# Kernel optimization log

Measured on AMD Instinct MI355X. Metric: run time of the kernel, lower is better.

## Reference

```python
import jax, jax.numpy as jnp
import numpy as np

B, C_COMB, HW_IN, HW_FEAT, N_POS, D_PROJ, OUT_HW = 32, 448, 32, 64, 4096, 100, 256


def setup_inputs() -> dict:
    key = jax.random.key(0)
    k1, k2, k3, k4 = jax.random.split(key, 4)
    return {
        "combined": jax.random.normal(k1, (B, C_COMB, HW_IN, HW_IN), dtype=jnp.float32),
        "proj_w": jax.random.normal(k2, (D_PROJ, C_COMB), dtype=jnp.float32),
        "proj_b": jnp.zeros((D_PROJ,), dtype=jnp.float32),
        "mean": jax.random.normal(k3, (D_PROJ, N_POS), dtype=jnp.float32),
        "inv_covariance": jax.random.normal(k4, (N_POS, D_PROJ, D_PROJ), dtype=jnp.float32),
        "norm_min": jnp.zeros((), dtype=jnp.float32),
        "norm_max": jnp.ones((), dtype=jnp.float32),
    }


def reference(combined, proj_w, proj_b, mean, inv_covariance, norm_min, norm_max):
    b = combined.shape[0]
    # F.interpolate(..., size=(64,64), mode='bilinear', align_corners=False)
    feats = jax.image.resize(combined, (b, C_COMB, HW_FEAT, HW_FEAT), method="bilinear")
    # permute to NHWC and flatten spatial -> [B, 4096, 448]
    feats = feats.transpose(0, 2, 3, 1).reshape(b, N_POS, C_COMB)
    # nn.Linear(channels, 100) -> [B, 4096, 100]
    feats = jnp.einsum("bnc,dc->bnd", feats, proj_w) + proj_b
    # per-pixel Mahalanobis quadratic form: diff_n^T @ Sigma_n^{-1} @ diff_n
    diff = feats - mean.T[None]                                  # [B, 4096, 100]
    dist = jnp.einsum("bnc,ncd,bnd->bn", diff, inv_covariance, diff)  # [B, 4096]
    anomaly_map = dist.reshape(b, 1, HW_FEAT, HW_FEAT)
    anomaly_map = (anomaly_map - norm_min) / (norm_max - norm_min + 1e-8)
    anomaly_map = jax.image.resize(anomaly_map, (b, 1, OUT_HW, OUT_HW), method="bilinear")
    return anomaly_map
```

## Files before the change

kernel.cpp:

```cpp
#include <hip/hip_runtime.h>

#define B_      32
#define C_COMB  448
#define N_POS_  4096
#define D_      100

typedef __attribute__((ext_vector_type(8))) short bf16x8;
typedef __attribute__((ext_vector_type(4))) float f32x4;

__device__ __forceinline__ unsigned short f2bf(float f) {
    unsigned u = __builtin_bit_cast(unsigned, f);
    u += 0x7FFFu + ((u >> 16) & 1u);
    return (unsigned short)(u >> 16);
}
__device__ __forceinline__ unsigned pack2bf(float a, float b) {
    return (unsigned)f2bf(a) | ((unsigned)f2bf(b) << 16);
}
__device__ __forceinline__ float bf2f(unsigned short h) {
    return __builtin_bit_cast(float, (unsigned)h << 16);
}
__device__ __forceinline__ float4 bf4_to_f4(uint2 u) {
    float4 r;
    r.x = __builtin_bit_cast(float, u.x << 16);
    r.y = __builtin_bit_cast(float, u.x & 0xffff0000u);
    r.z = __builtin_bit_cast(float, u.y << 16);
    r.w = __builtin_bit_cast(float, u.y & 0xffff0000u);
    return r;
}
__device__ __forceinline__ void async_copy16(const void* g, void* lds) {
    __builtin_amdgcn_global_load_lds(
        (const __attribute__((address_space(1))) unsigned int*)g,
        (__attribute__((address_space(3))) unsigned int*)lds, 16, 0, 0);
}
__device__ __forceinline__ bf16x8 pack8bf(float4 lo, float4 hi) {
    bf16x8 r;
    r[0] = (short)f2bf(lo.x); r[1] = (short)f2bf(lo.y);
    r[2] = (short)f2bf(lo.z); r[3] = (short)f2bf(lo.w);
    r[4] = (short)f2bf(hi.x); r[5] = (short)f2bf(hi.y);
    r[6] = (short)f2bf(hi.z); r[7] = (short)f2bf(hi.w);
    return r;
}

__global__ __launch_bounds__(256) void k_meanT(const float* __restrict__ mean,
                                               float* __restrict__ meanT) {
    int i = blockIdx.x * 256 + threadIdx.x;
    if (i < D_ * N_POS_) {
        int d = i >> 12;
        int n = i & 4095;
        meanT[n * D_ + d] = mean[i];
    }
}

__global__ __launch_bounds__(256) void k_combT(const float* __restrict__ comb,
                                               unsigned short* __restrict__ combT) {
    __shared__ float T_[64][65];
    const int pt = blockIdx.x;
    const int ct = blockIdx.y;
    const int b  = blockIdx.z;
    const int t  = threadIdx.x;
    const int c0 = ct * 64, p0 = pt * 64;

    const float4* comb4 = (const float4*)comb;
#pragma unroll
    for (int k = 0; k < 4; k++) {
        int e4 = t + 256 * k;
        int cc = e4 >> 4, p4 = e4 & 15;
        float4 v = comb4[(b * C_COMB + c0 + cc) * 256 + pt * 16 + p4];
        T_[cc][p4 * 4 + 0] = v.x;
        T_[cc][p4 * 4 + 1] = v.y;
        T_[cc][p4 * 4 + 2] = v.z;
        T_[cc][p4 * 4 + 3] = v.w;
    }
    __syncthreads();
#pragma unroll
    for (int k = 0; k < 4; k++) {
        int e4 = t + 256 * k;
        int pp = e4 >> 4, c4 = e4 & 15;
        float f0 = T_[c4 * 4 + 0][pp];
        float f1 = T_[c4 * 4 + 1][pp];
        float f2 = T_[c4 * 4 + 2][pp];
        float f3 = T_[c4 * 4 + 3][pp];
        size_t R = (size_t)(p0 + pp) * 32 + b;
        *(uint2*)(combT + R * C_COMB + c0 + c4 * 4) =
            make_uint2(pack2bf(f0, f1), pack2bf(f2, f3));
    }
}

__global__ __launch_bounds__(256) void k_proj(const unsigned short* __restrict__ combT,
                                              const float* __restrict__ W,
                                              const float* __restrict__ bias,
                                              unsigned short* __restrict__ p32b) {
    __shared__ unsigned short Bb[64 * C_COMB];
    __shared__ unsigned short Ab[D_ * 32];

    const int t = threadIdx.x;
    const int lane = t & 63, w = t >> 6;
    const int c = lane & 15, q = lane >> 4;
    const int R0 = blockIdx.x * 64;

    const unsigned short* gB = combT + (size_t)R0 * C_COMB;
#pragma unroll
    for (int k = 0; k < 14; k++) {
        int f4 = (k * 4 + w) * 64 + lane;
        async_copy16(gB + f4 * 8, Bb + f4 * 8);
    }

    f32x4 acc[7];
#pragma unroll
    for (int mt = 0; mt < 7; mt++) acc[mt] = (f32x4){0.f, 0.f, 0.f, 0.f};

    const float4* W4 = (const float4*)W;

    for (int kt = 0; kt < 14; kt++) {
        __syncthreads();
#pragma unroll
        for (int k = 0; k < 4; k++) {
            int e4 = t + 256 * k;
            if (e4 < 800) {
                int rr = e4 >> 3, c4 = e4 & 7;
                float4 v = W4[rr * 112 + kt * 8 + c4];
                *(uint2*)(Ab + rr * 32 + c4 * 4) =
                    make_uint2(pack2bf(v.x, v.y), pack2bf(v.z, v.w));
            }
        }
        __syncthreads();

        bf16x8 bfrag = *(const bf16x8*)(Bb + (w * 16 + c) * C_COMB + kt * 32 + q * 8);
#pragma unroll
        for (int mt = 0; mt < 7; mt++) {
            int r = mt * 16 + c;
            bf16x8 afrag;
            if (r < D_) afrag = *(const bf16x8*)(Ab + r * 32 + q * 8);
            else        afrag = (bf16x8){0,0,0,0,0,0,0,0};
            acc[mt] = __builtin_amdgcn_mfma_f32_16x16x32_bf16(afrag, bfrag, acc[mt], 0, 0, 0);
        }
    }

    const int R = R0 + w * 16 + c;
#pragma unroll
    for (int mt = 0; mt < 7; mt++) {
        int d0 = mt * 16 + q * 4;
        if (d0 < D_) {
            f32x4 a = acc[mt];
            float o0 = a[0] + bias[d0 + 0];
            float o1 = a[1] + bias[d0 + 1];
            float o2 = a[2] + bias[d0 + 2];
            float o3 = a[3] + bias[d0 + 3];
            *(uint2*)(p32b + (size_t)R * D_ + d0) =
                make_uint2(pack2bf(o0, o1), pack2bf(o2, o3));
        }
    }
}

__global__ __launch_bounds__(128) void k_mahal(const unsigned short* __restrict__ p32b,
                                               const float* __restrict__ meanT,
                                               const float* __restrict__ icov,
                                               float* __restrict__ gdist) {
    __shared__ float Mf[D_ * D_];
    __shared__ unsigned short dTb[B_ * 104];

    const int n = blockIdx.x;
    const int t = threadIdx.x;
    const int lane = t & 63, w = t >> 6;
    const int c = lane & 15, q = lane >> 4;

    const float* gM = icov + (size_t)n * (D_ * D_);
#pragma unroll
    for (int k = 0; k < 19; k++) {
        int f4 = k * 128 + w * 64 + lane;
        async_copy16(gM + f4 * 4, Mf + f4 * 4);
    }
    if (t < 68) {
        int f4 = 2432 + t;
        ((float4*)Mf)[f4] = ((const float4*)gM)[f4];
    }

    const int y = n >> 6, x = n & 63;
    float sy = 0.5f * y - 0.25f, sx = 0.5f * x - 0.25f;
    float y0f = floorf(sy), x0f = floorf(sx);
    float fy = sy - y0f, fx = sx - x0f;
    int iy0 = max((int)y0f, 0), iy1 = min((int)y0f + 1, 31);
    int ix0 = max((int)x0f, 0), ix1 = min((int)x0f + 1, 31);
    const float w00 = (1.f - fy) * (1.f - fx), w01 = (1.f - fy) * fx;
    const float w10 = fy * (1.f - fx),         w11 = fy * fx;
    const unsigned short* s00 = p32b + (size_t)(iy0 * 32 + ix0) * 3200;
    const unsigned short* s01 = p32b + (size_t)(iy0 * 32 + ix1) * 3200;
    const unsigned short* s10 = p32b + (size_t)(iy1 * 32 + ix0) * 3200;
    const unsigned short* s11 = p32b + (size_t)(iy1 * 32 + ix1) * 3200;

    const float4* mt4 = (const float4*)meanT + n * 25;
#pragma unroll
    for (int k = 0; k < 7; k++) {
        int e4 = t + 128 * k;
        if (e4 < 800) {
            int b  = e4 / 25;
            int d4 = e4 - b * 25;
            float4 f00 = bf4_to_f4(*(const uint2*)(s00 + e4 * 4));
            float4 f01 = bf4_to_f4(*(const uint2*)(s01 + e4 * 4));
            float4 f10 = bf4_to_f4(*(const uint2*)(s10 + e4 * 4));
            float4 f11 = bf4_to_f4(*(const uint2*)(s11 + e4 * 4));
            float4 m = mt4[d4];
            float vx = w00 * f00.x + w01 * f01.x + w10 * f10.x + w11 * f11.x - m.x;
            float vy = w00 * f00.y + w01 * f01.y + w10 * f10.y + w11 * f11.y - m.y;
            float vz = w00 * f00.z + w01 * f01.z + w10 * f10.z + w11 * f11.z - m.z;
            float vw = w00 * f00.w + w01 * f01.w + w10 * f10.w + w11 * f11.w - m.w;
            *(uint2*)(dTb + b * 104 + d4 * 4) =
                make_uint2(pack2bf(vx, vy), pack2bf(vz, vw));
        }
    }
    if (t < 32) *(uint2*)(dTb + t * 104 + 100) = make_uint2(0u, 0u);

    __syncthreads();

    const int bb = w * 16 + c;
    f32x4 acc[7];
#pragma unroll
    for (int mt = 0; mt < 7; mt++) acc[mt] = (f32x4){0.f, 0.f, 0.f, 0.f};

#pragma unroll
    for (int kt = 0; kt < 4; kt++) {
        int k0 = kt * 32 + q * 8;
        bf16x8 bfrag;
        if (k0 < 104) bfrag = *(const bf16x8*)(dTb + bb * 104 + k0);
        else          bfrag = (bf16x8){0,0,0,0,0,0,0,0};
#pragma unroll
        for (int mt = 0; mt < 7; mt++) {
            int r = mt * 16 + c;
            bf16x8 afrag;
            if (r < D_ && k0 < D_) {
                const float* src = Mf + r * D_ + k0;
                float4 lo = *(const float4*)(src);
                float4 hi;
                if (k0 + 7 < D_) hi = *(const float4*)(src + 4);
                else             hi = (float4){0.f, 0.f, 0.f, 0.f};
                afrag = pack8bf(lo, hi);
            } else {
                afrag = (bf16x8){0,0,0,0,0,0,0,0};
            }
            acc[mt] = __builtin_amdgcn_mfma_f32_16x16x32_bf16(afrag, bfrag, acc[mt], 0, 0, 0);
        }
    }

    float dist = 0.f;
#pragma unroll
    for (int mt = 0; mt < 7; mt++) {
#pragma unroll
        for (int reg = 0; reg < 4; reg++) {
            int r = mt * 16 + q * 4 + reg;
            if (r < D_) dist += acc[mt][reg] * bf2f(dTb[bb * 104 + r]);
        }
    }
    dist += __shfl_xor(dist, 16);
    dist += __shfl_xor(dist, 32);
    if (q == 0) gdist[bb * N_POS_ + n] = dist;
}

__global__ __launch_bounds__(256) void k_upsample(const float* __restrict__ gdist,
                                                  const float* __restrict__ nminp,
                                                  const float* __restrict__ nmaxp,
                                                  float* __restrict__ out) {
    int gid = blockIdx.x * 256 + threadIdx.x;
    int b   = gid >> 16;
    int rem = gid & 65535;
    int Y = rem >> 8, X = rem & 255;
    float sy = 0.25f * Y - 0.375f, sx = 0.25f * X - 0.375f;
    float y0f = floorf(sy), x0f = floorf(sx);
    float fy = sy - y0f, fx = sx - x0f;
    int iy0 = max((int)y0f, 0), iy1 = min((int)y0f + 1, 63);
    int ix0 = max((int)x0f, 0), ix1 = min((int)x0f + 1, 63);
    const float* g = gdist + b * N_POS_;
    float v00 = g[iy0 * 64 + ix0], v01 = g[iy0 * 64 + ix1];
    float v10 = g[iy1 * 64 + ix0], v11 = g[iy1 * 64 + ix1];
    float v = (1.f - fy) * ((1.f - fx) * v00 + fx * v01)
            +        fy  * ((1.f - fx) * v10 + fx * v11);
    float nmin = nminp[0], nmax = nmaxp[0];
    float scale = 1.0f / (nmax - nmin + 1e-8f);
    out[gid] = (v - nmin) * scale;
}

extern "C" void kernel_launch(void* const* d_in, const int* in_sizes, int n_in,
                              void* d_out, int out_size, void* d_ws, size_t ws_size,
                              hipStream_t stream) {
    const float* comb = (const float*)d_in[0];
    const float* W    = (const float*)d_in[1];
    const float* bias = (const float*)d_in[2];
    const float* mean = (const float*)d_in[3];
    const float* icov = (const float*)d_in[4];
    const float* nmin = (const float*)d_in[5];
    const float* nmax = (const float*)d_in[6];
    float* out = (float*)d_out;

    char* ws = (char*)d_ws;
    unsigned short* combT = (unsigned short*)(ws);
    float*          gdist = (float*)(ws);
    unsigned short* p32b  = (unsigned short*)(ws + 29360128);
    float*          meanT = (float*)(ws + 29360128 + 6553600);

    k_meanT   <<<1600, 256, 0, stream>>>(mean, meanT);
    k_combT   <<<dim3(16, 7, 32), 256, 0, stream>>>(comb, combT);
    k_proj    <<<512, 256, 0, stream>>>(combT, W, bias, p32b);
    k_mahal   <<<4096, 128, 0, stream>>>(p32b, meanT, icov, gdist);
    k_upsample<<<8192, 256, 0, stream>>>(gdist, nmin, nmax, out);
}
```

Baseline: 350.3 us.

## Fuse combined transpose into projection GEMM and split Mahalanobis across four waves

```diff
diff --git a/kernel.cpp b/kernel.cpp
--- a/kernel.cpp
+++ b/kernel.cpp
@@ -27,23 +27,16 @@
     r.w = __builtin_bit_cast(float, u.y & 0xffff0000u);
     return r;
 }
-__device__ __forceinline__ void async_copy16(const void* g, void* lds) {
-    __builtin_amdgcn_global_load_lds(
-        (const __attribute__((address_space(1))) unsigned int*)g,
-        (__attribute__((address_space(3))) unsigned int*)lds, 16, 0, 0);
-}
-__device__ __forceinline__ bf16x8 pack8bf(float4 lo, float4 hi) {
-    bf16x8 r;
-    r[0] = (short)f2bf(lo.x); r[1] = (short)f2bf(lo.y);
-    r[2] = (short)f2bf(lo.z); r[3] = (short)f2bf(lo.w);
-    r[4] = (short)f2bf(hi.x); r[5] = (short)f2bf(hi.y);
-    r[6] = (short)f2bf(hi.z); r[7] = (short)f2bf(hi.w);
-    return r;
-}
-
-__global__ __launch_bounds__(256) void k_meanT(const float* __restrict__ mean,
-                                               float* __restrict__ meanT) {
+
+__global__ __launch_bounds__(256) void k_prep(const float* __restrict__ W,
+                                              unsigned short* __restrict__ Wb,
+                                              const float* __restrict__ mean,
+                                              float* __restrict__ meanT) {
     int i = blockIdx.x * 256 + threadIdx.x;
+    if (i < 11200) {
+        float4 v = ((const float4*)W)[i];
+        ((uint2*)Wb)[i] = make_uint2(pack2bf(v.x, v.y), pack2bf(v.z, v.w));
+    }
     if (i < D_ * N_POS_) {
         int d = i >> 12;
         int n = i & 4095;
@@ -51,92 +44,63 @@
     }
 }
 
-__global__ __launch_bounds__(256) void k_combT(const float* __restrict__ comb,
-                                               unsigned short* __restrict__ combT) {
-    __shared__ float T_[64][65];
-    const int pt = blockIdx.x;
-    const int ct = blockIdx.y;
-    const int b  = blockIdx.z;
-    const int t  = threadIdx.x;
-    const int c0 = ct * 64, p0 = pt * 64;
-
-    const float4* comb4 = (const float4*)comb;
-#pragma unroll
-    for (int k = 0; k < 4; k++) {
-        int e4 = t + 256 * k;
-        int cc = e4 >> 4, p4 = e4 & 15;
-        float4 v = comb4[(b * C_COMB + c0 + cc) * 256 + pt * 16 + p4];
-        T_[cc][p4 * 4 + 0] = v.x;
-        T_[cc][p4 * 4 + 1] = v.y;
-        T_[cc][p4 * 4 + 2] = v.z;
-        T_[cc][p4 * 4 + 3] = v.w;
-    }
-    __syncthreads();
-#pragma unroll
-    for (int k = 0; k < 4; k++) {
-        int e4 = t + 256 * k;
-        int pp = e4 >> 4, c4 = e4 & 15;
-        float f0 = T_[c4 * 4 + 0][pp];
-        float f1 = T_[c4 * 4 + 1][pp];
-        float f2 = T_[c4 * 4 + 2][pp];
-        float f3 = T_[c4 * 4 + 3][pp];
-        size_t R = (size_t)(p0 + pp) * 32 + b;
-        *(uint2*)(combT + R * C_COMB + c0 + c4 * 4) =
-            make_uint2(pack2bf(f0, f1), pack2bf(f2, f3));
-    }
-}
-
-__global__ __launch_bounds__(256) void k_proj(const unsigned short* __restrict__ combT,
-                                              const float* __restrict__ W,
+__global__ __launch_bounds__(256) void k_proj(const float* __restrict__ comb,
+                                              const unsigned short* __restrict__ Wb,
                                               const float* __restrict__ bias,
                                               unsigned short* __restrict__ p32b) {
-    __shared__ unsigned short Bb[64 * C_COMB];
-    __shared__ unsigned short Ab[D_ * 32];
-
+    __shared__ float Tf[32 * 65];
+    __shared__ unsigned short Ws[D_ * 40];
+
+    const int pt = blockIdx.x, b = blockIdx.y;
     const int t = threadIdx.x;
     const int lane = t & 63, w = t >> 6;
     const int c = lane & 15, q = lane >> 4;
-    const int R0 = blockIdx.x * 64;
-
-    const unsigned short* gB = combT + (size_t)R0 * C_COMB;
-#pragma unroll
-    for (int k = 0; k < 14; k++) {
-        int f4 = (k * 4 + w) * 64 + lane;
-        async_copy16(gB + f4 * 8, Bb + f4 * 8);
-    }
 
     f32x4 acc[7];
 #pragma unroll
     for (int mt = 0; mt < 7; mt++) acc[mt] = (f32x4){0.f, 0.f, 0.f, 0.f};
 
-    const float4* W4 = (const float4*)W;
+    const float4* comb4 = (const float4*)comb;
 
     for (int kt = 0; kt < 14; kt++) {
         __syncthreads();
 #pragma unroll
+        for (int k = 0; k < 2; k++) {
+            int e4 = t + 256 * k;
+            int cc = e4 >> 4, p4 = e4 & 15;
+            float4 v = comb4[((size_t)b * C_COMB + kt * 32 + cc) * 256 + pt * 16 + p4];
+            Tf[cc * 65 + p4 * 4 + 0] = v.x;
+            Tf[cc * 65 + p4 * 4 + 1] = v.y;
+            Tf[cc * 65 + p4 * 4 + 2] = v.z;
+            Tf[cc * 65 + p4 * 4 + 3] = v.w;
+        }
+#pragma unroll
         for (int k = 0; k < 4; k++) {
-            int e4 = t + 256 * k;
-            if (e4 < 800) {
-                int rr = e4 >> 3, c4 = e4 & 7;
-                float4 v = W4[rr * 112 + kt * 8 + c4];
-                *(uint2*)(Ab + rr * 32 + c4 * 4) =
-                    make_uint2(pack2bf(v.x, v.y), pack2bf(v.z, v.w));
+            int e = t + 256 * k;
+            if (e < 800) {
+                int d = e >> 3, c4 = e & 7;
+                *(uint2*)(Ws + d * 40 + c4 * 4) =
+                    *(const uint2*)(Wb + d * C_COMB + kt * 32 + c4 * 4);
             }
         }
         __syncthreads();
 
-        bf16x8 bfrag = *(const bf16x8*)(Bb + (w * 16 + c) * C_COMB + kt * 32 + q * 8);
+        bf16x8 bfrag;
+#pragma unroll
+        for (int j = 0; j < 8; j++) {
+            bfrag[j] = (short)f2bf(Tf[(q * 8 + j) * 65 + w * 16 + c]);
+        }
 #pragma unroll
         for (int mt = 0; mt < 7; mt++) {
             int r = mt * 16 + c;
             bf16x8 afrag;
-            if (r < D_) afrag = *(const bf16x8*)(Ab + r * 32 + q * 8);
+            if (r < D_) afrag = *(const bf16x8*)(Ws + r * 40 + q * 8);
             else        afrag = (bf16x8){0,0,0,0,0,0,0,0};
             acc[mt] = __builtin_amdgcn_mfma_f32_16x16x32_bf16(afrag, bfrag, acc[mt], 0, 0, 0);
         }
     }
 
-    const int R = R0 + w * 16 + c;
+    const int pos = pt * 64 + w * 16 + c;
 #pragma unroll
     for (int mt = 0; mt < 7; mt++) {
         int d0 = mt * 16 + q * 4;
@@ -146,33 +110,38 @@
             float o1 = a[1] + bias[d0 + 1];
             float o2 = a[2] + bias[d0 + 2];
             float o3 = a[3] + bias[d0 + 3];
-            *(uint2*)(p32b + (size_t)R * D_ + d0) =
+            *(uint2*)(p32b + ((size_t)pos * B_ + b) * D_ + d0) =
                 make_uint2(pack2bf(o0, o1), pack2bf(o2, o3));
         }
     }
 }
 
-__global__ __launch_bounds__(128) void k_mahal(const unsigned short* __restrict__ p32b,
+__global__ __launch_bounds__(256) void k_mahal(const unsigned short* __restrict__ p32b,
                                                const float* __restrict__ meanT,
                                                const float* __restrict__ icov,
                                                float* __restrict__ gdist) {
-    __shared__ float Mf[D_ * D_];
+    __shared__ unsigned short Mb[D_ * 104];
     __shared__ unsigned short dTb[B_ * 104];
+    __shared__ float part[64];
 
     const int n = blockIdx.x;
     const int t = threadIdx.x;
     const int lane = t & 63, w = t >> 6;
     const int c = lane & 15, q = lane >> 4;
 
-    const float* gM = icov + (size_t)n * (D_ * D_);
-#pragma unroll
-    for (int k = 0; k < 19; k++) {
-        int f4 = k * 128 + w * 64 + lane;
-        async_copy16(gM + f4 * 4, Mf + f4 * 4);
-    }
-    if (t < 68) {
-        int f4 = 2432 + t;
-        ((float4*)Mf)[f4] = ((const float4*)gM)[f4];
+    if (t < 100) *(uint2*)(Mb + t * 104 + 100) = make_uint2(0u, 0u);
+    if (t >= 128 && t < 160) *(uint2*)(dTb + (t - 128) * 104 + 100) = make_uint2(0u, 0u);
+
+    const float4* gM4 = (const float4*)(icov + (size_t)n * (D_ * D_));
+#pragma unroll
+    for (int k = 0; k < 10; k++) {
+        int e4 = t + 256 * k;
+        if (e4 < 2500) {
+            float4 v = gM4[e4];
+            int r = e4 / 25, c4 = e4 - r * 25;
+            *(uint2*)(Mb + r * 104 + c4 * 4) =
+                make_uint2(pack2bf(v.x, v.y), pack2bf(v.z, v.w));
+        }
     }
 
     const int y = n >> 6, x = n & 63;
@@ -190,8 +159,8 @@
 
     const float4* mt4 = (const float4*)meanT + n * 25;
 #pragma unroll
-    for (int k = 0; k < 7; k++) {
-        int e4 = t + 128 * k;
+    for (int k = 0; k < 4; k++) {
+        int e4 = t + 256 * k;
         if (e4 < 800) {
             int b  = e4 / 25;
             int d4 = e4 - b * 25;
@@ -208,14 +177,14 @@
                 make_uint2(pack2bf(vx, vy), pack2bf(vz, vw));
         }
     }
-    if (t < 32) *(uint2*)(dTb + t * 104 + 100) = make_uint2(0u, 0u);
-
     __syncthreads();
 
-    const int bb = w * 16 + c;
-    f32x4 acc[7];
-#pragma unroll
-    for (int mt = 0; mt < 7; mt++) acc[mt] = (f32x4){0.f, 0.f, 0.f, 0.f};
+    const int g = w & 1, h = w >> 1;
+    const int bb = g * 16 + c;
+    const int mt0 = h * 4;
+    f32x4 acc[4];
+#pragma unroll
+    for (int mi = 0; mi < 4; mi++) acc[mi] = (f32x4){0.f, 0.f, 0.f, 0.f};
 
 #pragma unroll
     for (int kt = 0; kt < 4; kt++) {
@@ -224,35 +193,37 @@
         if (k0 < 104) bfrag = *(const bf16x8*)(dTb + bb * 104 + k0);
         else          bfrag = (bf16x8){0,0,0,0,0,0,0,0};
 #pragma unroll
-        for (int mt = 0; mt < 7; mt++) {
+        for (int mi = 0; mi < 4; mi++) {
+            int mt = mt0 + mi;
+            if (mt >= 7) continue;
             int r = mt * 16 + c;
             bf16x8 afrag;
-            if (r < D_ && k0 < D_) {
-                const float* src = Mf + r * D_ + k0;
-                float4 lo = *(const float4*)(src);
-                float4 hi;
-                if (k0 + 7 < D_) hi = *(const float4*)(src + 4);
-                else             hi = (float4){0.f, 0.f, 0.f, 0.f};
-                afrag = pack8bf(lo, hi);
-            } else {
-                afrag = (bf16x8){0,0,0,0,0,0,0,0};
-            }
-            acc[mt] = __builtin_amdgcn_mfma_f32_16x16x32_bf16(afrag, bfrag, acc[mt], 0, 0, 0);
+            if (r < D_ && k0 < 104) afrag = *(const bf16x8*)(Mb + r * 104 + k0);
+            else                    afrag = (bf16x8){0,0,0,0,0,0,0,0};
+            acc[mi] = __builtin_amdgcn_mfma_f32_16x16x32_bf16(afrag, bfrag, acc[mi], 0, 0, 0);
         }
     }
 
     float dist = 0.f;
 #pragma unroll
-    for (int mt = 0; mt < 7; mt++) {
+    for (int mi = 0; mi < 4; mi++) {
+        int mt = mt0 + mi;
+        if (mt >= 7) continue;
 #pragma unroll
         for (int reg = 0; reg < 4; reg++) {
             int r = mt * 16 + q * 4 + reg;
-            if (r < D_) dist += acc[mt][reg] * bf2f(dTb[bb * 104 + r]);
+            if (r < D_) dist += acc[mi][reg] * bf2f(dTb[bb * 104 + r]);
         }
     }
     dist += __shfl_xor(dist, 16);
     dist += __shfl_xor(dist, 32);
-    if (q == 0) gdist[bb * N_POS_ + n] = dist;
+    if (q == 0) part[w * 16 + c] = dist;
+    __syncthreads();
+    if (t < 32) {
+        int gg = t >> 4, cc = t & 15;
+        float s = part[gg * 16 + cc] + part[(gg + 2) * 16 + cc];
+        gdist[t * N_POS_ + n] = s;
+    }
 }
 
 __global__ __launch_bounds__(256) void k_upsample(const float* __restrict__ gdist,
@@ -291,14 +262,13 @@
     float* out = (float*)d_out;
 
     char* ws = (char*)d_ws;
-    unsigned short* combT = (unsigned short*)(ws);
-    float*          gdist = (float*)(ws);
-    unsigned short* p32b  = (unsigned short*)(ws + 29360128);
-    float*          meanT = (float*)(ws + 29360128 + 6553600);
-
-    k_meanT   <<<1600, 256, 0, stream>>>(mean, meanT);
-    k_combT   <<<dim3(16, 7, 32), 256, 0, stream>>>(comb, combT);
-    k_proj    <<<512, 256, 0, stream>>>(combT, W, bias, p32b);
-    k_mahal   <<<4096, 128, 0, stream>>>(p32b, meanT, icov, gdist);
+    unsigned short* p32b  = (unsigned short*)(ws);
+    float*          meanT = (float*)(ws + 6553600);
+    unsigned short* Wb    = (unsigned short*)(ws + 8192000);
+    float*          gdist = (float*)(ws + 8281600);
+
+    k_prep    <<<1600, 256, 0, stream>>>(W, Wb, mean, meanT);
+    k_proj    <<<dim3(16, 32), 256, 0, stream>>>(comb, Wb, bias, p32b);
+    k_mahal   <<<4096, 256, 0, stream>>>(p32b, meanT, icov, gdist);
     k_upsample<<<8192, 256, 0, stream>>>(gdist, nmin, nmax, out);
 }
```

Measured after the change: 317.1 us. 1.1x faster.
